# Kernel optimization log

Measured on AMD Instinct MI355X. Metric: run time of the kernel, lower is better.

## Reference

```python
import jax, jax.numpy as jnp
import numpy as np

N, D, L, K = 32, 128, 3136, 64

def setup_inputs() -> dict:
    key = jax.random.key(0)
    k1, k2, k3 = jax.random.split(key, 3)
    x = jax.random.normal(k1, (N, D, L), dtype=jnp.float32)
    weight = jax.random.normal(k2, (K, D), dtype=jnp.float32)  # codebook centers
    scale = jax.random.normal(k3, (1,), dtype=jnp.float32)
    return {"x": x, "weight": weight, "scale": scale}

def reference(x, weight, scale):
    # x: (N, C, ...) -> (N, D, L); output scaled squared L2 dist (N, K, L)
    n, c = x.shape[0], x.shape[1]
    xf = x.reshape(n, c, -1)  # (N, D, L)
    x_sq = jnp.sum(xf * xf, axis=1)          # (N, L)
    c_sq = jnp.sum(weight * weight, axis=1)  # (K,)
    xc = jnp.einsum('ndl,kd->nkl', xf, weight)  # (N, K, L)
    dist = x_sq[:, None, :] + c_sq[None, :, None] - 2.0 * xc
    return dist / (scale[0] ** 2)
```

## Files before the change

kernel.cpp:

```cpp
#include <hip/hip_runtime.h>

#define N_ 32
#define D_ 128
#define L_ 3136
#define K_ 64

typedef _Float16 f16x8 __attribute__((ext_vector_type(8)));
typedef float    f32x4 __attribute__((ext_vector_type(4)));

__global__ __launch_bounds__(64) void prep_kernel(
    const float* __restrict__ w,
    unsigned short* __restrict__ wh,
    float* __restrict__ csq)
{
    const int b = blockIdx.x, lane = threadIdx.x;
    if (b < 16) {
        const int dc = b >> 2, kt = b & 3;
        const int row = kt * 16 + (lane & 15);
        const int d0  = dc * 32 + (lane >> 4) * 8;
        const float* src = w + row * D_ + d0;
        __attribute__((aligned(16))) unsigned short h[8];
#pragma unroll
        for (int j = 0; j < 8; ++j) {
            _Float16 v = (_Float16)src[j];
            h[j] = *(const unsigned short*)&v;
        }
        const size_t off = (size_t)(b * 64 + lane) * 8;
        *(ushort4*)(wh + off)     = *(const ushort4*)(h);
        *(ushort4*)(wh + off + 4) = *(const ushort4*)(h + 4);
    } else {
        const float* wr = w + lane * D_;
        float s = 0.f;
#pragma unroll
        for (int d = 0; d < D_; d += 4) {
            float4 v = *(const float4*)(wr + d);
            s = fmaf(v.x, v.x, s); s = fmaf(v.y, v.y, s);
            s = fmaf(v.z, v.z, s); s = fmaf(v.w, v.w, s);
        }
        csq[lane] = s;
    }
}

__global__ __launch_bounds__(256, 6) void enc_mfma_kernel(
    const float* __restrict__ x,
    const unsigned short* __restrict__ wh,
    const float* __restrict__ csqg,
    const float* __restrict__ scale,
    float* __restrict__ out)
{
    __shared__ __attribute__((aligned(16))) unsigned short lds_w[8192];
    __shared__ float lds_csq[K_];

    const int t    = threadIdx.x;
    const int wave = t >> 6;
    const int lane = t & 63;
    const int col  = lane & 15;
    const int quad = lane >> 4;
    const int n    = blockIdx.y;
    const int l0   = blockIdx.x * 64;

#pragma unroll
    for (int i = 0; i < 4; ++i) {
        const int c = wave * 4 + i;
        __builtin_amdgcn_global_load_lds(
            (const __attribute__((address_space(1))) unsigned int*)(wh + (size_t)c * 512 + lane * 8),
            (__attribute__((address_space(3))) unsigned int*)&lds_w[c * 512],
            16, 0, 0);
    }
    if (wave == 0) {
        __builtin_amdgcn_global_load_lds(
            (const __attribute__((address_space(1))) unsigned int*)(csqg + lane),
            (__attribute__((address_space(3))) unsigned int*)lds_csq,
            4, 0, 0);
    }
    __syncthreads();

    const float* xa = x + (size_t)n * D_ * L_ + l0 + wave * 16 + col;

    f32x4 acc[4];
#pragma unroll
    for (int kt = 0; kt < 4; ++kt) acc[kt] = (f32x4){0.f, 0.f, 0.f, 0.f};
    float xsq = 0.f;

#pragma unroll
    for (int dc = 0; dc < 4; ++dc) {
        const float* xp = xa + (size_t)(dc * 32 + quad * 8) * L_;
        float xv[8];
#pragma unroll
        for (int j = 0; j < 8; ++j) xv[j] = xp[(size_t)j * L_];

        union { f16x8 v; _Float16 e[8]; } af;
#pragma unroll
        for (int j = 0; j < 8; ++j) {
            xsq = fmaf(xv[j], xv[j], xsq);
            af.e[j] = (_Float16)xv[j];
        }

#pragma unroll
        for (int kt = 0; kt < 4; ++kt) {
            const int fo = ((dc * 4 + kt) * 64 + lane) * 8;
            f16x8 bf = *(const f16x8*)&lds_w[fo];
            acc[kt] = __builtin_amdgcn_mfma_f32_16x16x32_f16(af.v, bf, acc[kt], 0, 0, 0);
        }
    }

    xsq += __shfl_xor(xsq, 16, 64);
    xsq += __shfl_xor(xsq, 32, 64);
    float xs[4];
#pragma unroll
    for (int r = 0; r < 4; ++r)
        xs[r] = __shfl(xsq, quad * 4 + r, 64);

    const float sc = scale[0];
    const float inv_s2 = 1.0f / (sc * sc);
    float* op = out + (size_t)n * K_ * L_ + l0 + wave * 16 + quad * 4;
#pragma unroll
    for (int kt = 0; kt < 4; ++kt) {
        const float cs = lds_csq[kt * 16 + col];
        float4 v;
        v.x = (xs[0] + cs - 2.0f * acc[kt][0]) * inv_s2;
        v.y = (xs[1] + cs - 2.0f * acc[kt][1]) * inv_s2;
        v.z = (xs[2] + cs - 2.0f * acc[kt][2]) * inv_s2;
        v.w = (xs[3] + cs - 2.0f * acc[kt][3]) * inv_s2;
        *(float4*)(op + (size_t)(kt * 16 + col) * L_) = v;
    }
}

extern "C" void kernel_launch(void* const* d_in, const int* in_sizes, int n_in,
                              void* d_out, int out_size, void* d_ws, size_t ws_size,
                              hipStream_t stream) {
    const float* x     = (const float*)d_in[0];
    const float* w     = (const float*)d_in[1];
    const float* scale = (const float*)d_in[2];
    float* out = (float*)d_out;

    unsigned short* wh  = (unsigned short*)d_ws;
    float*          csq = (float*)((char*)d_ws + 16384);

    prep_kernel<<<17, 64, 0, stream>>>(w, wh, csq);
    dim3 grid(L_ / 64, N_);
    enc_mfma_kernel<<<grid, 256, 0, stream>>>(x, wh, csq, scale, out);
}
```

Before: 97.90 us.

## Stage x tile through LDS with async global_load_lds and split-phase waits

Instead of each lane doing strided scalar global loads of x, the block now issues 16-byte global_load_lds transfers of the whole 128x64 x tile into a swizzled LDS buffer. It then waits in two phases so the first half of the D dimension can be computed while the second half is still arriving. The goal is fully coalesced vector reads and overlap of load latency with MFMA work. The extra 32KB of LDS lowers the occupancy hint from 6 to 3 blocks per CU, which may reduce latency hiding across blocks.

```diff
diff --git a/kernel.cpp b/kernel.cpp
--- a/kernel.cpp
+++ b/kernel.cpp
@@ -41,13 +41,14 @@
     }
 }
 
-__global__ __launch_bounds__(256, 6) void enc_mfma_kernel(
+__global__ __launch_bounds__(256, 3) void enc_mfma_kernel(
     const float* __restrict__ x,
     const unsigned short* __restrict__ wh,
     const float* __restrict__ csqg,
     const float* __restrict__ scale,
     float* __restrict__ out)
 {
+    __shared__ __attribute__((aligned(16))) float lds_x[8192];
     __shared__ __attribute__((aligned(16))) unsigned short lds_w[8192];
     __shared__ float lds_csq[K_];
 
@@ -73,33 +74,69 @@
             (__attribute__((address_space(3))) unsigned int*)lds_csq,
             4, 0, 0);
     }
-    __syncthreads();
 
-    const float* xa = x + (size_t)n * D_ * L_ + l0 + wave * 16 + col;
+    const float* xn = x + (size_t)n * D_ * L_ + l0;
+#pragma unroll
+    for (int i = 0; i < 8; ++i) {
+        const int cid = i * 256 + t;
+        const int d   = cid >> 4;
+        const int lg  = (cid & 15) ^ (((d >> 3) & 3) << 2);
+        __builtin_amdgcn_global_load_lds(
+            (const __attribute__((address_space(1))) unsigned int*)(xn + (size_t)d * L_ + lg * 4),
+            (__attribute__((address_space(3))) unsigned int*)&lds_x[i * 1024 + wave * 256],
+            16, 0, 0);
+    }
 
     f32x4 acc[4];
 #pragma unroll
     for (int kt = 0; kt < 4; ++kt) acc[kt] = (f32x4){0.f, 0.f, 0.f, 0.f};
     float xsq = 0.f;
 
+    const int wl    = wave * 16 + col;
+    const int lbase = (((wl >> 2) ^ (quad << 2)) << 2) | (col & 3);
+
+    asm volatile("s_waitcnt vmcnt(4)" ::: "memory");
+    __builtin_amdgcn_s_barrier();
+    __builtin_amdgcn_sched_barrier(0);
+
 #pragma unroll
-    for (int dc = 0; dc < 4; ++dc) {
-        const float* xp = xa + (size_t)(dc * 32 + quad * 8) * L_;
+    for (int dc = 0; dc < 2; ++dc) {
+        const float* xp = &lds_x[(dc * 32 + quad * 8) * 64 + lbase];
         float xv[8];
 #pragma unroll
-        for (int j = 0; j < 8; ++j) xv[j] = xp[(size_t)j * L_];
-
+        for (int j = 0; j < 8; ++j) xv[j] = xp[j * 64];
         union { f16x8 v; _Float16 e[8]; } af;
 #pragma unroll
         for (int j = 0; j < 8; ++j) {
             xsq = fmaf(xv[j], xv[j], xsq);
             af.e[j] = (_Float16)xv[j];
         }
+#pragma unroll
+        for (int kt = 0; kt < 4; ++kt) {
+            f16x8 bf = *(const f16x8*)&lds_w[((dc * 4 + kt) * 64 + lane) * 8];
+            acc[kt] = __builtin_amdgcn_mfma_f32_16x16x32_f16(af.v, bf, acc[kt], 0, 0, 0);
+        }
+    }
+
+    asm volatile("s_waitcnt vmcnt(0)" ::: "memory");
+    __builtin_amdgcn_s_barrier();
+    __builtin_amdgcn_sched_barrier(0);
 
 #pragma unroll
+    for (int dc = 2; dc < 4; ++dc) {
+        const float* xp = &lds_x[(dc * 32 + quad * 8) * 64 + lbase];
+        float xv[8];
+#pragma unroll
+        for (int j = 0; j < 8; ++j) xv[j] = xp[j * 64];
+        union { f16x8 v; _Float16 e[8]; } af;
+#pragma unroll
+        for (int j = 0; j < 8; ++j) {
+            xsq = fmaf(xv[j], xv[j], xsq);
+            af.e[j] = (_Float16)xv[j];
+        }
+#pragma unroll
         for (int kt = 0; kt < 4; ++kt) {
-            const int fo = ((dc * 4 + kt) * 64 + lane) * 8;
-            f16x8 bf = *(const f16x8*)&lds_w[fo];
+            f16x8 bf = *(const f16x8*)&lds_w[((dc * 4 + kt) * 64 + lane) * 8];
             acc[kt] = __builtin_amdgcn_mfma_f32_16x16x32_f16(af.v, bf, acc[kt], 0, 0, 0);
         }
     }
```

Measured after the change: 98.47 us. Within noise of the previous version (+0.6%).
